# Kernel optimization log

Measured on AMD Instinct MI355X. Metric: run time of the kernel, lower is better.

Reference implementation:

```python
import jax, jax.numpy as jnp
import numpy as np

B, S, H, NH = 4, 2048, 256, 8
EPS = 1e-5


def setup_inputs() -> dict:
    key = jax.random.key(0)
    ks = jax.random.split(key, 12)
    p = lambda k, shape: (jax.random.normal(k, shape, jnp.float32) * 0.02)
    return {
        "x": jax.random.normal(ks[0], (B, S, H), jnp.float32),
        "lengths": jax.random.randint(ks[1], (B,), 0, S).astype(jnp.int32),
        "atten_in": jnp.zeros((1,), jnp.float32),
        "Wq": p(ks[2], (H, H)), "bq": jnp.zeros((H,), jnp.float32),
        "Wk": p(ks[3], (H, H)), "bk": jnp.zeros((H,), jnp.float32),
        "Wv": p(ks[4], (H, H)), "bv": jnp.zeros((H,), jnp.float32),
        "W1": p(ks[5], (H, H)), "b1": jnp.zeros((H,), jnp.float32),
        "W2": p(ks[6], (H, H)), "b2": jnp.zeros((H,), jnp.float32),
        "g1": jnp.ones((H,), jnp.float32), "beta1": jnp.zeros((H,), jnp.float32),
        "g2": jnp.ones((H,), jnp.float32), "beta2": jnp.zeros((H,), jnp.float32),
    }


def _layer_norm(x, g, b):
    mu = x.mean(-1, keepdims=True)
    var = ((x - mu) ** 2).mean(-1, keepdims=True)
    return (x - mu) / jnp.sqrt(var + EPS) * g + b


def reference(x, lengths, atten_in, Wq, bq, Wk, bk, Wv, bv, W1, b1, W2, b2, g1, beta1, g2, beta2):
    Bx, Sx, Hx = x.shape
    hd = Hx // NH
    # QKV projections, split heads -> [B, NH, S, hd]
    q = (x @ Wq + bq).reshape(Bx, Sx, NH, hd).transpose(0, 2, 1, 3)
    k = (x @ Wk + bk).reshape(Bx, Sx, NH, hd).transpose(0, 2, 1, 3)
    v = (x @ Wv + bv).reshape(Bx, Sx, NH, hd).transpose(0, 2, 1, 3)
    # NOTE: original scales by sqrt(hidden_size), not sqrt(head_dim)
    scores = jnp.einsum('bhqd,bhkd->bhqk', q, k) / np.sqrt(Hx).astype(np.float32)
    pos = jnp.arange(Sx)
    causal = pos[:, None] >= pos[None, :]                     # [S, S]
    row_ok = pos[None, :] < lengths[:, None]                  # [B, S]: mask query rows >= length
    head_ok = jnp.arange(NH)[None, :] < lengths[:, None]      # [B, NH]: original loop masks heads >= length
    mask = causal[None, None] & row_ok[:, None, :, None] & head_ok[:, :, None, None]
    neg = jnp.finfo(scores.dtype).min
    logits = jnp.where(mask, scores, neg)
    atten = jax.nn.softmax(logits, axis=-1)
    # original: masked_fill((atten > 0) == False, 0) -> fully masked rows (NaN in torch) become 0
    atten = jnp.where(mask, atten, 0.0)
    row_valid = mask.any(-1, keepdims=True)
    atten = jnp.where(row_valid, atten, 0.0)
    out = jnp.einsum('bhqk,bhkd->bhqd', atten, v).transpose(0, 2, 1, 3).reshape(Bx, Sx, Hx)
    atten_mean = atten.mean(axis=1)  # [B, S, S], detached in original
    out_1 = x + out  # dropout p=0 / eval mode -> identity
    out_1_norm = _layer_norm(out_1, g1, beta1)
    ff = jax.nn.gelu(out_1_norm @ W1 + b1, approximate=False) @ W2 + b2
    y_prim = _layer_norm(out_1_norm + ff, g2, beta2)
    return (y_prim, lengths, atten_mean)
```

## Files before the change

### kernel.cpp

```cpp
#include <hip/hip_runtime.h>
#include <math.h>

#define BB 4
#define SS 2048
#define HH 256
#define NHH 8
#define EPSV 1e-5f
#define NC 8
#define CHW (SS/NC)
#define NCO 4
#define QPRE 0.09016844005556021f

#if __has_builtin(__builtin_amdgcn_exp2f)
#define EXP2F(x) __builtin_amdgcn_exp2f(x)
#else
#define EXP2F(x) __expf((x) * 0.6931471805599453f)
#endif

typedef unsigned short ushortT;
typedef __attribute__((ext_vector_type(8))) short bf16x8;
typedef __attribute__((ext_vector_type(4))) float f32x4;

__device__ inline ushortT f2bf(float f) {
    union { float f; unsigned int u; } x; x.f = f;
    unsigned int r = x.u + 0x7FFFu + ((x.u >> 16) & 1u);
    return (ushortT)(r >> 16);
}
__device__ inline ushortT f2bf_rz(float f) {
    union { float f; unsigned int u; } x; x.f = f;
    return (ushortT)(x.u >> 16);
}
__device__ inline float bf2f(ushortT u) {
    union { unsigned int i; float f; } x; x.i = ((unsigned int)u) << 16;
    return x.f;
}

__global__ __launch_bounds__(256) void prep(const int* __restrict__ L,
        float* __restrict__ out_len,
        const float* __restrict__ Wa, const float* __restrict__ Wb,
        const float* __restrict__ Wc, const float* __restrict__ Wd,
        const float* __restrict__ We, ushortT* __restrict__ Wtb) {
    const int wb = blockIdx.x;
    if (wb == 0 && threadIdx.x < BB) out_len[threadIdx.x] = (float)L[threadIdx.x];
    const int z = wb >> 6;
    const int rem = wb & 63;
    const int k0 = (rem >> 3) << 5, n0 = (rem & 7) << 5;
    const float* W = (z == 0) ? Wa : (z == 1) ? Wb : (z == 2) ? Wc : (z == 3) ? Wd : We;
    __shared__ float tile[32][33];
    const int t = threadIdx.x;
    const int r = t >> 3, c4 = (t & 7) << 2;
    float4 v = *(const float4*)(W + (size_t)(k0 + r) * HH + n0 + c4);
    tile[r][c4+0] = v.x; tile[r][c4+1] = v.y; tile[r][c4+2] = v.z; tile[r][c4+3] = v.w;
    __syncthreads();
    ushort4 o;
    o.x = f2bf(tile[c4+0][r]); o.y = f2bf(tile[c4+1][r]);
    o.z = f2bf(tile[c4+2][r]); o.w = f2bf(tile[c4+3][r]);
    *(ushort4*)(Wtb + (size_t)z * 65536 + (size_t)(n0 + r) * HH + k0 + c4) = o;
}

__global__ __launch_bounds__(256) void gemm_qkv(const float* __restrict__ X,
        const ushortT* __restrict__ Wtb,
        const float* __restrict__ bq, const float* __restrict__ bk,
        const float* __restrict__ bv,
        ushortT* __restrict__ Qb, ushortT* __restrict__ Kb,
        ushortT* __restrict__ Vt) {
    __shared__ ushortT As[64][264];
    __shared__ ushortT Ws[64][264];
    const int wsel = blockIdx.y >> 2;
    const int n0 = (blockIdx.y & 3) << 6;
    const ushortT* Wt = Wtb + (size_t)wsel * 65536;
    const float* bias = (wsel == 0) ? bq : (wsel == 1) ? bk : bv;
    const int tid = threadIdx.x;
    const int m0 = blockIdx.x << 6;
    #pragma unroll
    for (int t = 0; t < 8; ++t) {
        const int f = t * 256 + tid;
        const int r = f >> 5;
        const int cc = (f & 31) << 3;
        const float* xrow = X + (size_t)(m0 + r) * HH + cc;
        float4 v0 = *(const float4*)xrow;
        float4 v1 = *(const float4*)(xrow + 4);
        bf16x8 o;
        o[0] = (short)f2bf(v0.x); o[1] = (short)f2bf(v0.y);
        o[2] = (short)f2bf(v0.z); o[3] = (short)f2bf(v0.w);
        o[4] = (short)f2bf(v1.x); o[5] = (short)f2bf(v1.y);
        o[6] = (short)f2bf(v1.z); o[7] = (short)f2bf(v1.w);
        *(bf16x8*)&As[r][cc] = o;
        *(bf16x8*)&Ws[r][cc] = *(const bf16x8*)(Wt + (size_t)(n0 + r) * HH + cc);
    }
    __syncthreads();
    const int w = tid >> 6, lane = tid & 63;
    const int lg = lane >> 4, lc = lane & 15;
    const int wr = (w & 1) << 5, wc = (w >> 1) << 5;
    f32x4 acc[2][2];
    const f32x4 z4 = {0.f, 0.f, 0.f, 0.f};
    acc[0][0] = z4; acc[0][1] = z4; acc[1][0] = z4; acc[1][1] = z4;
    #pragma unroll
    for (int k0 = 0; k0 < 256; k0 += 32) {
        bf16x8 a0 = *(const bf16x8*)&As[wr + lc][k0 + lg*8];
        bf16x8 a1 = *(const bf16x8*)&As[wr + 16 + lc][k0 + lg*8];
        bf16x8 b0 = *(const bf16x8*)&Ws[wc + lc][k0 + lg*8];
        bf16x8 b1 = *(const bf16x8*)&Ws[wc + 16 + lc][k0 + lg*8];
        acc[0][0] = __builtin_amdgcn_mfma_f32_16x16x32_bf16(a0, b0, acc[0][0], 0, 0, 0);
        acc[0][1] = __builtin_amdgcn_mfma_f32_16x16x32_bf16(a0, b1, acc[0][1], 0, 0, 0);
        acc[1][0] = __builtin_amdgcn_mfma_f32_16x16x32_bf16(a1, b0, acc[1][0], 0, 0, 0);
        acc[1][1] = __builtin_amdgcn_mfma_f32_16x16x32_bf16(a1, b1, acc[1][1], 0, 0, 0);
    }
    ushortT* Out = (wsel == 0) ? Qb : Kb;
    #pragma unroll
    for (int RH = 0; RH < 2; ++RH)
        #pragma unroll
        for (int CH = 0; CH < 2; ++CH) {
            const int col = n0 + wc + CH*16 + lc;
            const float bvv = bias[col];
            float v[4];
            #pragma unroll
            for (int r = 0; r < 4; ++r) {
                v[r] = acc[RH][CH][r] + bvv;
                if (wsel == 0) v[r] *= QPRE;
            }
            if (wsel < 2) {
                #pragma unroll
                for (int r = 0; r < 4; ++r) {
                    const int row = m0 + wr + RH*16 + lg*4 + r;
                    Out[(size_t)row * HH + col] = f2bf(v[r]);
                }
            } else {
                const int row0 = m0 + wr + RH*16 + lg*4;
                const int bidx = row0 >> 11, s0 = row0 & (SS - 1);
                ushort4 o;
                o.x = f2bf(v[0]); o.y = f2bf(v[1]); o.z = f2bf(v[2]); o.w = f2bf(v[3]);
                *(ushort4*)(Vt + ((size_t)(bidx * HH + col)) * SS + s0) = o;
            }
        }
}

__global__ __launch_bounds__(512) void ln_ffn1(const float* __restrict__ x,
        const ushortT* __restrict__ OPart, const int* __restrict__ lengths,
        const float* __restrict__ g, const float* __restrict__ beta,
        const ushortT* __restrict__ W1t, const float* __restrict__ b1,
        float* __restrict__ X1N, ushortT* __restrict__ F1b) {
    __shared__ ushortT Ws[256][264];
    __shared__ ushortT As[32][264];
    const int tid = threadIdx.x;
    const int m0 = blockIdx.x << 5;
    #pragma unroll
    for (int t = 0; t < 16; ++t) {
        const int f = t * 512 + tid;
        const int r = f >> 5;
        const int cc = (f & 31) << 3;
        *(bf16x8*)&Ws[r][cc] = *(const bf16x8*)(W1t + (size_t)r * HH + cc);
    }
    const int w = tid >> 6, lane = tid & 63;
    const int lg = lane >> 4, lc = lane & 15;
    const int len = lengths[m0 >> 11];
    const int col0 = lane << 2;
    #pragma unroll
    for (int rr = 0; rr < 4; ++rr) {
        const int row = m0 + w * 4 + rr;
        const int i = row & (SS - 1);
        const size_t base = (size_t)row * HH;
        float4 v = *(const float4*)(x + base + col0);
        if (i < len) {
            const int ncv = min(NCO, (i >> 5) + 1);
            for (int cc = 0; cc < ncv; ++cc) {
                ushort4 o = *(const ushort4*)(OPart +
                    (size_t)cc * ((size_t)BB * SS * HH) + base + col0);
                v.x += bf2f(o.x); v.y += bf2f(o.y);
                v.z += bf2f(o.z); v.w += bf2f(o.w);
            }
        }
        float s = v.x + v.y + v.z + v.w;
        #pragma unroll
        for (int o = 1; o < 64; o <<= 1) s += __shfl_xor(s, o);
        const float mu = s * 0.00390625f;
        float4 d = make_float4(v.x - mu, v.y - mu, v.z - mu, v.w - mu);
        float q = d.x*d.x + d.y*d.y + d.z*d.z + d.w*d.w;
        #pragma unroll
        for (int o = 1; o < 64; o <<= 1) q += __shfl_xor(q, o);
        const float rs = rsqrtf(q * 0.00390625f + EPSV);
        float4 res;
        res.x = d.x * rs * g[col0+0] + beta[col0+0];
        res.y = d.y * rs * g[col0+1] + beta[col0+1];
        res.z = d.z * rs * g[col0+2] + beta[col0+2];
        res.w = d.w * rs * g[col0+3] + beta[col0+3];
        *(float4*)(X1N + base + col0) = res;
        ushort4 rb;
        rb.x = f2bf(res.x); rb.y = f2bf(res.y);
        rb.z = f2bf(res.z); rb.w = f2bf(res.w);
        *(ushort4*)&As[w * 4 + rr][col0] = rb;
    }
    __syncthreads();
    const int n0 = (w >> 1) << 6;
    const int ch = (w & 1) << 5;
    f32x4 acc[2][2];
    const f32x4 z4 = {0.f, 0.f, 0.f, 0.f};
    acc[0][0] = z4; acc[0][1] = z4; acc[1][0] = z4; acc[1][1] = z4;
    #pragma unroll
    for (int k0 = 0; k0 < 256; k0 += 32) {
        bf16x8 a0 = *(const bf16x8*)&As[lc][k0 + lg*8];
        bf16x8 a1 = *(const bf16x8*)&As[16 + lc][k0 + lg*8];
        bf16x8 b0 = *(const bf16x8*)&Ws[n0 + ch + lc][k0 + lg*8];
        bf16x8 b1 = *(const bf16x8*)&Ws[n0 + ch + 16 + lc][k0 + lg*8];
        acc[0][0] = __builtin_amdgcn_mfma_f32_16x16x32_bf16(a0, b0, acc[0][0], 0, 0, 0);
        acc[0][1] = __builtin_amdgcn_mfma_f32_16x16x32_bf16(a0, b1, acc[0][1], 0, 0, 0);
        acc[1][0] = __builtin_amdgcn_mfma_f32_16x16x32_bf16(a1, b0, acc[1][0], 0, 0, 0);
        acc[1][1] = __builtin_amdgcn_mfma_f32_16x16x32_bf16(a1, b1, acc[1][1], 0, 0, 0);
    }
    #pragma unroll
    for (int RH = 0; RH < 2; ++RH)
        #pragma unroll
        for (int CH = 0; CH < 2; ++CH) {
            const int col = n0 + ch + CH*16 + lc;
            const float bv = b1[col];
            #pragma unroll
            for (int r = 0; r < 4; ++r) {
                const int row = m0 + RH*16 + lg*4 + r;
                float v = acc[RH][CH][r] + bv;
                v = 0.5f * v * (1.0f + erff(v * 0.70710678118f));
                F1b[(size_t)row * HH + col] = f2bf(v);
            }
        }
}

__global__ __launch_bounds__(512) void ffn2_ln(const ushortT* __restrict__ A,
        const ushortT* __restrict__ W2t, const float* __restrict__ b2,
        const float* __restrict__ X1N, const float* __restrict__ g,
        const float* __restrict__ be, float* __restrict__ out) {
    __shared__ ushortT Ws[256][264];
    __shared__ ushortT As[32][264];
    __shared__ float redA[8][32];
    __shared__ float redB[8][32];
    const int tid = threadIdx.x;
    const int m0 = blockIdx.x << 5;
    #pragma unroll
    for (int t = 0; t < 16; ++t) {
        const int f = t * 512 + tid;
        const int r = f >> 5;
        const int cc = (f & 31) << 3;
        *(bf16x8*)&Ws[r][cc] = *(const bf16x8*)(W2t + (size_t)r * HH + cc);
    }
    #pragma unroll
    for (int t = 0; t < 2; ++t) {
        const int f = t * 512 + tid;
        const int r = f >> 5;
        const int cc = (f & 31) << 3;
        *(bf16x8*)&As[r][cc] = *(const bf16x8*)(A + (size_t)(m0 + r) * HH + cc);
    }
    __syncthreads();
    const int w = tid >> 6, lane = tid & 63;
    const int lg = lane >> 4, lc = lane & 15;
    const int n0 = (w >> 1) << 6;
    const int ch = (w & 1) << 5;
    f32x4 acc[2][2];
    const f32x4 z4 = {0.f, 0.f, 0.f, 0.f};
    acc[0][0] = z4; acc[0][1] = z4; acc[1][0] = z4; acc[1][1] = z4;
    #pragma unroll
    for (int k0 = 0; k0 < 256; k0 += 32) {
        bf16x8 a0 = *(const bf16x8*)&As[lc][k0 + lg*8];
        bf16x8 a1 = *(const bf16x8*)&As[16 + lc][k0 + lg*8];
        bf16x8 b0 = *(const bf16x8*)&Ws[n0 + ch + lc][k0 + lg*8];
        bf16x8 b1 = *(const bf16x8*)&Ws[n0 + ch + 16 + lc][k0 + lg*8];
        acc[0][0] = __builtin_amdgcn_mfma_f32_16x16x32_bf16(a0, b0, acc[0][0], 0, 0, 0);
        acc[0][1] = __builtin_amdgcn_mfma_f32_16x16x32_bf16(a0, b1, acc[0][1], 0, 0, 0);
        acc[1][0] = __builtin_amdgcn_mfma_f32_16x16x32_bf16(a1, b0, acc[1][0], 0, 0, 0);
        acc[1][1] = __builtin_amdgcn_mfma_f32_16x16x32_bf16(a1, b1, acc[1][1], 0, 0, 0);
    }
    float v[2][2][4];
    float rs[2][4] = {};
    #pragma unroll
    for (int RH = 0; RH < 2; ++RH)
        #pragma unroll
        for (int CH = 0; CH < 2; ++CH) {
            const int col = n0 + ch + CH*16 + lc;
            const float bv = b2[col];
            #pragma unroll
            for (int r = 0; r < 4; ++r) {
                const int row = m0 + RH*16 + lg*4 + r;
                float vv = acc[RH][CH][r] + bv + X1N[(size_t)row * HH + col];
                v[RH][CH][r] = vv;
                rs[RH][r] += vv;
            }
        }
    #pragma unroll
    for (int RH = 0; RH < 2; ++RH)
        #pragma unroll
        for (int r = 0; r < 4; ++r) {
            rs[RH][r] += __shfl_xor(rs[RH][r], 1);
            rs[RH][r] += __shfl_xor(rs[RH][r], 2);
            rs[RH][r] += __shfl_xor(rs[RH][r], 4);
            rs[RH][r] += __shfl_xor(rs[RH][r], 8);
        }
    if (lc == 0) {
        #pragma unroll
        for (int RH = 0; RH < 2; ++RH)
            #pragma unroll
            for (int r = 0; r < 4; ++r)
                redA[w][RH*16 + lg*4 + r] = rs[RH][r];
    }
    __syncthreads();
    float mu[2][4];
    #pragma unroll
    for (int RH = 0; RH < 2; ++RH)
        #pragma unroll
        for (int r = 0; r < 4; ++r) {
            const int rl = RH*16 + lg*4 + r;
            mu[RH][r] = (redA[0][rl] + redA[1][rl] + redA[2][rl] + redA[3][rl]
                       + redA[4][rl] + redA[5][rl] + redA[6][rl] + redA[7][rl])
                      * 0.00390625f;
        }
    float qs[2][4] = {};
    #pragma unroll
    for (int RH = 0; RH < 2; ++RH)
        #pragma unroll
        for (int CH = 0; CH < 2; ++CH)
            #pragma unroll
            for (int r = 0; r < 4; ++r) {
                const float d = v[RH][CH][r] - mu[RH][r];
                qs[RH][r] += d * d;
            }
    #pragma unroll
    for (int RH = 0; RH < 2; ++RH)
        #pragma unroll
        for (int r = 0; r < 4; ++r) {
            qs[RH][r] += __shfl_xor(qs[RH][r], 1);
            qs[RH][r] += __shfl_xor(qs[RH][r], 2);
            qs[RH][r] += __shfl_xor(qs[RH][r], 4);
            qs[RH][r] += __shfl_xor(qs[RH][r], 8);
        }
    if (lc == 0) {
        #pragma unroll
        for (int RH = 0; RH < 2; ++RH)
            #pragma unroll
            for (int r = 0; r < 4; ++r)
                redB[w][RH*16 + lg*4 + r] = qs[RH][r];
    }
    __syncthreads();
    #pragma unroll
    for (int RH = 0; RH < 2; ++RH)
        #pragma unroll
        for (int r = 0; r < 4; ++r) {
            const int rl = RH*16 + lg*4 + r;
            const float var = (redB[0][rl] + redB[1][rl] + redB[2][rl] + redB[3][rl]
                             + redB[4][rl] + redB[5][rl] + redB[6][rl] + redB[7][rl])
                            * 0.00390625f;
            const float rq = rsqrtf(var + EPSV);
            const int row = m0 + rl;
            #pragma unroll
            for (int CH = 0; CH < 2; ++CH) {
                const int col = n0 + ch + CH*16 + lc;
                out[(size_t)row * HH + col] =
                    (v[RH][CH][r] - mu[RH][r]) * rq * g[col] + be[col];
            }
        }
}

__global__ __launch_bounds__(512) void attn_sums(const ushortT* __restrict__ Qb,
        const ushortT* __restrict__ Kb, const int* __restrict__ lengths,
        float* __restrict__ Psum, float* __restrict__ out_mean) {
    const int b = blockIdx.z, c = blockIdx.y;
    const int i0 = (63 - blockIdx.x) << 5;
    const int len = lengths[b];
    const int tid = threadIdx.x;
    const int w = tid >> 6, lane = tid & 63;
    const int T = (i0 < len) ? ((min(i0 + 31, len - 1) >> 5) + 1) : 0;
    {
        const int zs = max(T * 32 - c * CHW, 0);
        if (zs < CHW) {
            #pragma unroll
            for (int rr = 0; rr < 4; ++rr) {
                float* mrow = out_mean + ((size_t)(b * SS + i0 + w * 4 + rr)) * SS + c * CHW;
                const int col = zs + (lane << 2);
                if (col < CHW)
                    *(float4*)(mrow + col) = make_float4(0.f, 0.f, 0.f, 0.f);
            }
        }
    }
    const int jmax = min(i0 + 31, len - 1);
    const int jstart = c * CHW;
    if (i0 >= len || jstart > jmax) return;
    const int lg = lane >> 4, lc = lane & 15;
    bf16x8 qf[2];
    #pragma unroll
    for (int RH = 0; RH < 2; ++RH)
        qf[RH] = *(const bf16x8*)(Qb + ((size_t)(b * SS + i0 + RH*16 + lc)) * HH + w*32 + lg*8);
    const f32x4 z4 = {0.f, 0.f, 0.f, 0.f};
    float lsum[2][4] = {};
    const int jend = min(jstart + CHW - 32, (jmax >> 5) << 5);
    bf16x8 kf0 = *(const bf16x8*)(Kb + ((size_t)(b * SS + jstart + lc)) * HH + w*32 + lg*8);
    bf16x8 kf1 = *(const bf16x8*)(Kb + ((size_t)(b * SS + jstart + 16 + lc)) * HH + w*32 + lg*8);
    for (int j0 = jstart; j0 <= jend; j0 += 32) {
        bf16x8 ck0 = kf0, ck1 = kf1;
        if (j0 + 32 <= jend) {
            kf0 = *(const bf16x8*)(Kb + ((size_t)(b * SS + j0 + 32 + lc)) * HH + w*32 + lg*8);
            kf1 = *(const bf16x8*)(Kb + ((size_t)(b * SS + j0 + 48 + lc)) * HH + w*32 + lg*8);
        }
        f32x4 s[2][2];
        #pragma unroll
        for (int RH = 0; RH < 2; ++RH) {
            s[RH][0] = __builtin_amdgcn_mfma_f32_16x16x32_bf16(qf[RH], ck0, z4, 0, 0, 0);
            s[RH][1] = __builtin_amdgcn_mfma_f32_16x16x32_bf16(qf[RH], ck1, z4, 0, 0, 0);
        }
        if (j0 < i0) {
            #pragma unroll
            for (int RH = 0; RH < 2; ++RH)
                #pragma unroll
                for (int r = 0; r < 4; ++r)
                    #pragma unroll
                    for (int CH = 0; CH < 2; ++CH)
                        lsum[RH][r] += EXP2F(s[RH][CH][r]);
        } else {
            #pragma unroll
            for (int RH = 0; RH < 2; ++RH)
                #pragma unroll
                for (int r = 0; r < 4; ++r) {
                    const int row = i0 + RH*16 + lg*4 + r;
                    #pragma unroll
                    for (int CH = 0; CH < 2; ++CH) {
                        const int j = j0 + CH*16 + lc;
                        lsum[RH][r] += (j <= row) ? EXP2F(s[RH][CH][r]) : 0.f;
                    }
                }
        }
    }
    #pragma unroll
    for (int RH = 0; RH < 2; ++RH)
        #pragma unroll
        for (int r = 0; r < 4; ++r) {
            float v = lsum[RH][r];
            v += __shfl_xor(v, 1); v += __shfl_xor(v, 2);
            v += __shfl_xor(v, 4); v += __shfl_xor(v, 8);
            if (lc == 0)
                Psum[((size_t)(c * BB + b) * NHH + w) * SS + i0 + RH*16 + lg*4 + r] = v;
        }
}

__global__ __launch_bounds__(512) void attn_pv(const ushortT* __restrict__ Qb,
        const ushortT* __restrict__ Kb, const ushortT* __restrict__ Vt,
        const int* __restrict__ lengths, const float* __restrict__ Psum,
        ushortT* __restrict__ OPart, float* __restrict__ out_mean) {
    __shared__ __align__(16) ushortT Pb[2][NHH][32][40];
    __shared__ float invS[NHH][32];
    const int b = blockIdx.z, cg = blockIdx.y;
    const int i0 = (63 - blockIdx.x) << 5;
    const int len = lengths[b];
    const int tid = threadIdx.x;
    const int mr = tid >> 4, mc = (tid & 15) << 1;
    float* meanrow = out_mean + ((size_t)(b * SS + i0 + mr)) * SS + mc;
    const int T = (i0 < len) ? ((min(i0 + 31, len - 1) >> 5) + 1) : 0;
    const int q = T >> 2, r = T & (NCO - 1);
    const int t0 = cg * q + min(cg, r);
    const int t1 = t0 + q + (cg < r ? 1 : 0);
    if (t0 >= t1) return;
    if (tid < NHH * 32) {
        const int hh = tid >> 5, row = i0 + (tid & 31);
        float rv = 0.f;
        if (row < len && hh < len) {
            float s = 0.f;
            const int ncv = (row >> 8) + 1;
            for (int c2 = 0; c2 < ncv; ++c2)
                s += Psum[((size_t)(c2 * BB + b) * NHH + hh) * SS + row];
            rv = (s > 0.f) ? 1.0f / s : 0.f;
        }
        invS[hh][tid & 31] = rv;
    }
    __syncthreads();
    const int w = tid >> 6, lane = tid & 63;
    const int lg = lane >> 4, lc = lane & 15;
    bf16x8 qf[2];
    #pragma unroll
    for (int RH = 0; RH < 2; ++RH)
        qf[RH] = *(const bf16x8*)(Qb + ((size_t)(b * SS + i0 + RH*16 + lc)) * HH + w*32 + lg*8);
    float invv[2][4];
    #pragma unroll
    for (int RH = 0; RH < 2; ++RH)
        #pragma unroll
        for (int r2 = 0; r2 < 4; ++r2)
            invv[RH][r2] = invS[w][RH*16 + lg*4 + r2];
    float invh8[NHH];
    #pragma unroll
    for (int hh = 0; hh < NHH; ++hh)
        invh8[hh] = invS[hh][mr] * 0.125f;
    const f32x4 z4 = {0.f, 0.f, 0.f, 0.f};
    f32x4 O[2][2];
    O[0][0] = z4; O[0][1] = z4; O[1][0] = z4; O[1][1] = z4;
    const int jstart = t0 << 5;
    bf16x8 kf0 = *(const bf16x8*)(Kb + ((size_t)(b * SS + jstart + lc)) * HH + w*32 + lg*8);
    bf16x8 kf1 = *(const bf16x8*)(Kb + ((size_t)(b * SS + jstart + 16 + lc)) * HH + w*32 + lg*8);
    bf16x8 vf0 = *(const bf16x8*)(Vt + ((size_t)(b * HH + w*32 + lc)) * SS + jstart + lg*8);
    bf16x8 vf1 = *(const bf16x8*)(Vt + ((size_t)(b * HH + w*32 + 16 + lc)) * SS + jstart + lg*8);
    for (int t = t0; t < t1; ++t) {
        const int j0 = t << 5;
        const int par = t & 1;
        bf16x8 ck0 = kf0, ck1 = kf1, cv0 = vf0, cv1 = vf1;
        if (t + 1 < t1) {
            kf0 = *(const bf16x8*)(Kb + ((size_t)(b * SS + j0 + 32 + lc)) * HH + w*32 + lg*8);
            kf1 = *(const bf16x8*)(Kb + ((size_t)(b * SS + j0 + 48 + lc)) * HH + w*32 + lg*8);
            vf0 = *(const bf16x8*)(Vt + ((size_t)(b * HH + w*32 + lc)) * SS + j0 + 32 + lg*8);
            vf1 = *(const bf16x8*)(Vt + ((size_t)(b * HH + w*32 + 16 + lc)) * SS + j0 + 32 + lg*8);
        }
        f32x4 s[2][2];
        #pragma unroll
        for (int RH = 0; RH < 2; ++RH) {
            s[RH][0] = __builtin_amdgcn_mfma_f32_16x16x32_bf16(qf[RH], ck0, z4, 0, 0, 0);
            s[RH][1] = __builtin_amdgcn_mfma_f32_16x16x32_bf16(qf[RH], ck1, z4, 0, 0, 0);
        }
        if (j0 < i0) {
            #pragma unroll
            for (int RH = 0; RH < 2; ++RH)
                #pragma unroll
                for (int CH = 0; CH < 2; ++CH)
                    #pragma unroll
                    for (int r2 = 0; r2 < 4; ++r2)
                        Pb[par][w][RH*16 + lg*4 + r2][CH*16 + lc] =
                            f2bf_rz(EXP2F(s[RH][CH][r2]));
        } else {
            #pragma unroll
            for (int RH = 0; RH < 2; ++RH)
                #pragma unroll
                for (int CH = 0; CH < 2; ++CH)
                    #pragma unroll
                    for (int r2 = 0; r2 < 4; ++r2) {
                        const int row = i0 + RH*16 + lg*4 + r2;
                        const int j = j0 + CH*16 + lc;
                        Pb[par][w][RH*16 + lg*4 + r2][CH*16 + lc] =
                            (j <= row) ? f2bf_rz(EXP2F(s[RH][CH][r2])) : (ushortT)0;
                    }
        }
        #pragma unroll
        for (int RH = 0; RH < 2; ++RH) {
            bf16x8 pa = *(const bf16x8*)&Pb[par][w][RH*16 + lc][lg*8];
            O[RH][0] = __builtin_amdgcn_mfma_f32_16x16x32_bf16(pa, cv0, O[RH][0], 0, 0, 0);
            O[RH][1] = __builtin_amdgcn_mfma_f32_16x16x32_bf16(pa, cv1, O[RH][1], 0, 0, 0);
        }
        __syncthreads();
        float m0 = 0.f, m1 = 0.f;
        #pragma unroll
        for (int ww = 0; ww < NHH; ++ww) {
            ushort2 t2 = *(const ushort2*)&Pb[par][ww][mr][mc];
            m0 += bf2f(t2.x) * invh8[ww]; m1 += bf2f(t2.y) * invh8[ww];
        }
        *(float2*)(meanrow + j0) = make_float2(m0, m1);
    }
    ushortT* op = OPart + (size_t)cg * ((size_t)BB * SS * HH);
    #pragma unroll
    for (int RH = 0; RH < 2; ++RH)
        #pragma unroll
        for (int DH = 0; DH < 2; ++DH)
            #pragma unroll
            for (int r2 = 0; r2 < 4; ++r2)
                op[((size_t)(b * SS + i0 + RH*16 + lg*4 + r2)) * HH + w*32 + DH*16 + lc] =
                    f2bf(O[RH][DH][r2] * invv[RH][r2]);
}

extern "C" void kernel_launch(void* const* d_in, const int* in_sizes, int n_in,
                              void* d_out, int out_size, void* d_ws, size_t ws_size,
                              hipStream_t stream) {
    const float* x   = (const float*)d_in[0];
    const int* lengths = (const int*)d_in[1];
    const float* Wq  = (const float*)d_in[3];
    const float* bq  = (const float*)d_in[4];
    const float* Wk  = (const float*)d_in[5];
    const float* bk  = (const float*)d_in[6];
    const float* Wv  = (const float*)d_in[7];
    const float* bv  = (const float*)d_in[8];
    const float* W1  = (const float*)d_in[9];
    const float* b1  = (const float*)d_in[10];
    const float* W2  = (const float*)d_in[11];
    const float* b2  = (const float*)d_in[12];
    const float* g1  = (const float*)d_in[13];
    const float* be1 = (const float*)d_in[14];
    const float* g2  = (const float*)d_in[15];
    const float* be2 = (const float*)d_in[16];
    float* out = (float*)d_out;
    float* ws  = (float*)d_ws;

    const size_t NELT = (size_t)BB * SS * HH;
    const size_t M1 = 1024 * 1024;

    float*   Psum = ws;
    ushortT* Qbf = (ushortT*)(ws + M1);
    ushortT* Kbf = (ushortT*)(ws + 2 * M1);
    ushortT* Vtb = (ushortT*)(ws + 3 * M1);
    float*   X1N  = ws + 4 * M1;
    ushortT* Wtb = (ushortT*)(ws + 6 * M1);
    ushortT* OPart = (ushortT*)(ws + 7 * M1);
    ushortT* F1b  = (ushortT*)(ws + M1);

    float* out_y    = out;
    float* out_len  = out + NELT;
    float* out_mean = out + NELT + 4;

    prep<<<320, 256, 0, stream>>>(lengths, out_len, Wq, Wk, Wv, W1, W2, Wtb);
    gemm_qkv<<<dim3(128, 12), 256, 0, stream>>>(x, Wtb, bq, bk, bv, Qbf, Kbf, Vtb);
    attn_sums<<<dim3(64, NC, 4), 512, 0, stream>>>(Qbf, Kbf, lengths, Psum, out_mean);
    attn_pv<<<dim3(64, NCO, 4), 512, 0, stream>>>(Qbf, Kbf, Vtb, lengths, Psum, OPart, out_mean);
    ln_ffn1<<<256, 512, 0, stream>>>(x, OPart, lengths, g1, be1,
                                     Wtb + 3 * 65536, b1, X1N, F1b);
    ffn2_ln<<<256, 512, 0, stream>>>(F1b, Wtb + 4 * 65536, b2, X1N, g2, be2, out_y);
}
```

Measured before the change: 94.87 us.

## Fuse LN1+FFN1 and FFN2+LN2 kernels, keeping GELU activations in shared memory

Merges the two FFN kernels into one block-level kernel. The GELU output is written to shared memory as bf16 and the W2 weights are reloaded into the same shared buffer, so the F1 intermediate no longer goes through global memory. This drops one kernel launch and the 4 MB global write and read of F1. X1N is still written and then read back by the same block. The W2 load now runs serially after the first GEMM inside each block, with no overlap.

```diff
diff --git a/kernel.cpp b/kernel.cpp
--- a/kernel.cpp
+++ b/kernel.cpp
@@ -135,13 +135,17 @@
         }
 }
 
-__global__ __launch_bounds__(512) void ln_ffn1(const float* __restrict__ x,
+__global__ __launch_bounds__(512) void ffn_fused(const float* __restrict__ x,
         const ushortT* __restrict__ OPart, const int* __restrict__ lengths,
-        const float* __restrict__ g, const float* __restrict__ beta,
+        const float* __restrict__ g1, const float* __restrict__ be1,
         const ushortT* __restrict__ W1t, const float* __restrict__ b1,
-        float* __restrict__ X1N, ushortT* __restrict__ F1b) {
+        const ushortT* __restrict__ W2t, const float* __restrict__ b2,
+        const float* __restrict__ g2, const float* __restrict__ be2,
+        float* __restrict__ X1N, float* __restrict__ out) {
     __shared__ ushortT Ws[256][264];
     __shared__ ushortT As[32][264];
+    __shared__ float redA[8][32];
+    __shared__ float redB[8][32];
     const int tid = threadIdx.x;
     const int m0 = blockIdx.x << 5;
     #pragma unroll
@@ -180,10 +184,10 @@
         for (int o = 1; o < 64; o <<= 1) q += __shfl_xor(q, o);
         const float rs = rsqrtf(q * 0.00390625f + EPSV);
         float4 res;
-        res.x = d.x * rs * g[col0+0] + beta[col0+0];
-        res.y = d.y * rs * g[col0+1] + beta[col0+1];
-        res.z = d.z * rs * g[col0+2] + beta[col0+2];
-        res.w = d.w * rs * g[col0+3] + beta[col0+3];
+        res.x = d.x * rs * g1[col0+0] + be1[col0+0];
+        res.y = d.y * rs * g1[col0+1] + be1[col0+1];
+        res.z = d.z * rs * g1[col0+2] + be1[col0+2];
+        res.w = d.w * rs * g1[col0+3] + be1[col0+3];
         *(float4*)(X1N + base + col0) = res;
         ushort4 rb;
         rb.x = f2bf(res.x); rb.y = f2bf(res.y);
@@ -211,28 +215,21 @@
     for (int RH = 0; RH < 2; ++RH)
         #pragma unroll
         for (int CH = 0; CH < 2; ++CH) {
-            const int col = n0 + ch + CH*16 + lc;
-            const float bv = b1[col];
+            const float bv = b1[n0 + ch + CH*16 + lc];
             #pragma unroll
             for (int r = 0; r < 4; ++r) {
-                const int row = m0 + RH*16 + lg*4 + r;
                 float v = acc[RH][CH][r] + bv;
-                v = 0.5f * v * (1.0f + erff(v * 0.70710678118f));
-                F1b[(size_t)row * HH + col] = f2bf(v);
-            }
-        }
-}
-
-__global__ __launch_bounds__(512) void ffn2_ln(const ushortT* __restrict__ A,
-        const ushortT* __restrict__ W2t, const float* __restrict__ b2,
-        const float* __restrict__ X1N, const float* __restrict__ g,
-        const float* __restrict__ be, float* __restrict__ out) {
-    __shared__ ushortT Ws[256][264];
-    __shared__ ushortT As[32][264];
-    __shared__ float redA[8][32];
-    __shared__ float redB[8][32];
-    const int tid = threadIdx.x;
-    const int m0 = blockIdx.x << 5;
+                acc[RH][CH][r] = 0.5f * v * (1.0f + erff(v * 0.70710678118f));
+            }
+        }
+    __syncthreads();
+    #pragma unroll
+    for (int RH = 0; RH < 2; ++RH)
+        #pragma unroll
+        for (int CH = 0; CH < 2; ++CH)
+            #pragma unroll
+            for (int r = 0; r < 4; ++r)
+                As[RH*16 + lg*4 + r][n0 + ch + CH*16 + lc] = f2bf(acc[RH][CH][r]);
     #pragma unroll
     for (int t = 0; t < 16; ++t) {
         const int f = t * 512 + tid;
@@ -240,20 +237,7 @@
         const int cc = (f & 31) << 3;
         *(bf16x8*)&Ws[r][cc] = *(const bf16x8*)(W2t + (size_t)r * HH + cc);
     }
-    #pragma unroll
-    for (int t = 0; t < 2; ++t) {
-        const int f = t * 512 + tid;
-        const int r = f >> 5;
-        const int cc = (f & 31) << 3;
-        *(bf16x8*)&As[r][cc] = *(const bf16x8*)(A + (size_t)(m0 + r) * HH + cc);
-    }
-    __syncthreads();
-    const int w = tid >> 6, lane = tid & 63;
-    const int lg = lane >> 4, lc = lane & 15;
-    const int n0 = (w >> 1) << 6;
-    const int ch = (w & 1) << 5;
-    f32x4 acc[2][2];
-    const f32x4 z4 = {0.f, 0.f, 0.f, 0.f};
+    __syncthreads();
     acc[0][0] = z4; acc[0][1] = z4; acc[1][0] = z4; acc[1][1] = z4;
     #pragma unroll
     for (int k0 = 0; k0 < 256; k0 += 32) {
@@ -267,7 +251,7 @@
         acc[1][1] = __builtin_amdgcn_mfma_f32_16x16x32_bf16(a1, b1, acc[1][1], 0, 0, 0);
     }
     float v[2][2][4];
-    float rs[2][4] = {};
+    float rs2[2][4] = {};
     #pragma unroll
     for (int RH = 0; RH < 2; ++RH)
         #pragma unroll
@@ -279,35 +263,35 @@
                 const int row = m0 + RH*16 + lg*4 + r;
                 float vv = acc[RH][CH][r] + bv + X1N[(size_t)row * HH + col];
                 v[RH][CH][r] = vv;
-                rs[RH][r] += vv;
+                rs2[RH][r] += vv;
             }
         }
     #pragma unroll
     for (int RH = 0; RH < 2; ++RH)
         #pragma unroll
         for (int r = 0; r < 4; ++r) {
-            rs[RH][r] += __shfl_xor(rs[RH][r], 1);
-            rs[RH][r] += __shfl_xor(rs[RH][r], 2);
-            rs[RH][r] += __shfl_xor(rs[RH][r], 4);
-            rs[RH][r] += __shfl_xor(rs[RH][r], 8);
+            rs2[RH][r] += __shfl_xor(rs2[RH][r], 1);
+            rs2[RH][r] += __shfl_xor(rs2[RH][r], 2);
+            rs2[RH][r] += __shfl_xor(rs2[RH][r], 4);
+            rs2[RH][r] += __shfl_xor(rs2[RH][r], 8);
         }
     if (lc == 0) {
         #pragma unroll
         for (int RH = 0; RH < 2; ++RH)
             #pragma unroll
             for (int r = 0; r < 4; ++r)
-                redA[w][RH*16 + lg*4 + r] = rs[RH][r];
-    }
-    __syncthreads();
-    float mu[2][4];
+                redA[w][RH*16 + lg*4 + r] = rs2[RH][r];
+    }
+    __syncthreads();
+    float mu2[2][4];
     #pragma unroll
     for (int RH = 0; RH < 2; ++RH)
         #pragma unroll
         for (int r = 0; r < 4; ++r) {
             const int rl = RH*16 + lg*4 + r;
-            mu[RH][r] = (redA[0][rl] + redA[1][rl] + redA[2][rl] + redA[3][rl]
-                       + redA[4][rl] + redA[5][rl] + redA[6][rl] + redA[7][rl])
-                      * 0.00390625f;
+            mu2[RH][r] = (redA[0][rl] + redA[1][rl] + redA[2][rl] + redA[3][rl]
+                        + redA[4][rl] + redA[5][rl] + redA[6][rl] + redA[7][rl])
+                       * 0.00390625f;
         }
     float qs[2][4] = {};
     #pragma unroll
@@ -316,7 +300,7 @@
         for (int CH = 0; CH < 2; ++CH)
             #pragma unroll
             for (int r = 0; r < 4; ++r) {
-                const float d = v[RH][CH][r] - mu[RH][r];
+                const float d = v[RH][CH][r] - mu2[RH][r];
                 qs[RH][r] += d * d;
             }
     #pragma unroll
@@ -350,7 +334,7 @@
             for (int CH = 0; CH < 2; ++CH) {
                 const int col = n0 + ch + CH*16 + lc;
                 out[(size_t)row * HH + col] =
-                    (v[RH][CH][r] - mu[RH][r]) * rq * g[col] + be[col];
+                    (v[RH][CH][r] - mu2[RH][r]) * rq * g2[col] + be2[col];
             }
         }
 }
@@ -585,7 +569,6 @@
     float*   X1N  = ws + 4 * M1;
     ushortT* Wtb = (ushortT*)(ws + 6 * M1);
     ushortT* OPart = (ushortT*)(ws + 7 * M1);
-    ushortT* F1b  = (ushortT*)(ws + M1);
 
     float* out_y    = out;
     float* out_len  = out + NELT;
@@ -595,7 +578,7 @@
     gemm_qkv<<<dim3(128, 12), 256, 0, stream>>>(x, Wtb, bq, bk, bv, Qbf, Kbf, Vtb);
     attn_sums<<<dim3(64, NC, 4), 512, 0, stream>>>(Qbf, Kbf, lengths, Psum, out_mean);
     attn_pv<<<dim3(64, NCO, 4), 512, 0, stream>>>(Qbf, Kbf, Vtb, lengths, Psum, OPart, out_mean);
-    ln_ffn1<<<256, 512, 0, stream>>>(x, OPart, lengths, g1, be1,
-                                     Wtb + 3 * 65536, b1, X1N, F1b);
-    ffn2_ln<<<256, 512, 0, stream>>>(F1b, Wtb + 4 * 65536, b2, X1N, g2, be2, out_y);
-}
+    ffn_fused<<<256, 512, 0, stream>>>(x, OPart, lengths, g1, be1,
+                                       Wtb + 3 * 65536, b1, Wtb + 4 * 65536, b2,
+                                       g2, be2, X1N, out_y);
+}
```

Result: faster. 91.30 us (-3.8%).
